# Performance work log

Measured on AMD Instinct MI355X. Metric: run time of the kernel, lower is better.

The kernel has to match this reference:

```python
import jax, jax.numpy as jnp
import numpy as np

N = 200000
SIZE = 16384
IN = 128
OUT = 128
HEADS = 4
SLOPE = 0.01  # nn.LeakyReLU default


def setup_inputs() -> dict:
    key = jax.random.key(0)
    ks = jax.random.split(key, 12)
    s = 0.05
    inp = {
        "fea": jax.random.normal(ks[0], (N, IN), jnp.float32),
        "cry_fea": jax.random.normal(ks[1], (SIZE, IN), jnp.float32),
        # MH_M: per-head MLP in->in->out (grouped conv1d k=1, groups=heads)
        "W_m1": jax.random.normal(ks[2], (HEADS, IN, IN), jnp.float32) * s,
        "b_m1": jax.random.normal(ks[3], (HEADS, IN), jnp.float32) * s,
        "W_m2": jax.random.normal(ks[4], (HEADS, OUT, IN), jnp.float32) * s,
        "b_m2": jax.random.normal(ks[5], (HEADS, OUT), jnp.float32) * s,
        # MH_A: per-head MLP 2*in->in->1 (scalar attention, vector_attention=False)
        "W_a1": jax.random.normal(ks[6], (HEADS, IN, 2 * IN), jnp.float32) * s,
        "b_a1": jax.random.normal(ks[7], (HEADS, IN), jnp.float32) * s,
        "W_a2": jax.random.normal(ks[8], (HEADS, 1, IN), jnp.float32) * s,
        "b_a2": jax.random.normal(ks[9], (HEADS, 1), jnp.float32) * s,
        "index": jnp.sort(jax.random.randint(ks[10], (N,), 0, SIZE, jnp.int32)),
        "size": SIZE,
    }
    return inp


def _leaky(x):
    return jnp.where(x >= 0, x, SLOPE * x)


def _mh_mlp(x, W1, b1, W2, b2):
    # x: [N, d_in]; per-head linear -> leaky -> linear. Returns [N, H, d_out].
    h = _leaky(jnp.einsum("ni,hoi->nho", x, W1) + b1)
    return jnp.einsum("nhi,hoi->nho", h, W2) + b2


def reference(fea, cry_fea, W_m1, b_m1, W_m2, b_m2, W_a1, b_a1, W_a2, b_a2, index, size):
    # message transform m: [N, H, OUT]
    m = _mh_mlp(fea, W_m1, b_m1, W_m2, b_m2)
    # attention input: concat(node fea, gathered crystal fea) -> [N, 2*IN]
    a_in = jnp.concatenate([fea, cry_fea[index]], axis=-1)
    alpha = _mh_mlp(a_in, W_a1, b_a1, W_a2, b_a2)  # [N, H, 1]
    # segment (per-crystal) softmax over nodes sharing the same index
    amax = jax.ops.segment_max(alpha, index, num_segments=size)
    amax = jnp.where(jnp.isfinite(amax), amax, 0.0)
    e = jnp.exp(alpha - amax[index])
    denom = jax.ops.segment_sum(e, index, num_segments=size)
    alpha = e / (denom[index] + 1e-16)
    # weighted scatter-add aggregation -> [size, H*OUT]
    out = jax.ops.segment_sum((alpha * m).reshape(-1, HEADS * OUT), index, num_segments=size)
    return out
```

## Files before the change

kernel.cpp:

```cpp
#include <hip/hip_runtime.h>

typedef __bf16 bf16x8 __attribute__((ext_vector_type(8)));
typedef float  f32x4  __attribute__((ext_vector_type(4)));
typedef unsigned int u32x4 __attribute__((ext_vector_type(4)));

#define MFMA(a, b, c) __builtin_amdgcn_mfma_f32_16x16x32_bf16((a), (b), (c), 0, 0, 0)

#define THREADS 1024
#define WAVES   16
#define CPW     4
#define CPB     64
#define MT      32

#define SEG_INTS  16416
#define SEG_BYTES (SEG_INTS * 4)
#define O_WM1 0
#define O_WM2 65536
#define O_WA1 131072
#define O_WA2 262144
#define W_ELEMS 262656
#define W_BYTES (W_ELEMS * 2)

#define LA1B 0
#define LM1B 32768
#define LM2B 65536

__device__ __forceinline__ bf16x8 cvt8(const float* pf) {
    float4 a = *(const float4*)pf, b = *(const float4*)(pf + 4);
    bf16x8 o;
    o[0] = (__bf16)a.x; o[1] = (__bf16)a.y; o[2] = (__bf16)a.z; o[3] = (__bf16)a.w;
    o[4] = (__bf16)b.x; o[5] = (__bf16)b.y; o[6] = (__bf16)b.z; o[7] = (__bf16)b.w;
    return o;
}

__device__ __forceinline__ unsigned pk2(float a, float b) {
    unsigned short ua = __builtin_bit_cast(unsigned short, (__bf16)a);
    unsigned short ub = __builtin_bit_cast(unsigned short, (__bf16)b);
    return (unsigned)ua | ((unsigned)ub << 16);
}

__device__ __forceinline__ int lower_bound(const int* __restrict__ a, int n, int v) {
    int lo = 0, hi = n;
    while (lo < hi) { int mid = (lo + hi) >> 1; if (a[mid] < v) lo = mid + 1; else hi = mid; }
    return lo;
}

__global__ __launch_bounds__(256) void prep3_kernel(
    const float* __restrict__ Wm1, const float* __restrict__ Wm2,
    const float* __restrict__ Wa1, const float* __restrict__ Wa2,
    const float* __restrict__ fea, const float* __restrict__ cry,
    const int* __restrict__ index, int N, int S,
    int segBlocks, int packBlocks, int cryBlocks,
    int* __restrict__ seg, __bf16* __restrict__ wb,
    __bf16* __restrict__ cryb, __bf16* __restrict__ feab, int full)
{
    int b = blockIdx.x;
    if (b < segBlocks) {
        int c = b * 256 + threadIdx.x;
        if (c <= S) seg[c] = lower_bound(index, N, c);
        return;
    }
    if (!full) return;
    b -= segBlocks;
    if (b < packBlocks) {
        int i8 = b * 256 + threadIdx.x;
        if (i8 >= W_ELEMS / 8) return;
        int i = i8 * 8;
        const float* src; int s;
        if      (i < O_WM2) { src = Wm1; s = i; }
        else if (i < O_WA1) { src = Wm2; s = i - O_WM2; }
        else if (i < O_WA2) { src = Wa1; s = i - O_WA1; }
        else                { src = Wa2; s = i - O_WA2; }
        *(bf16x8*)(wb + i) = cvt8(src + s);
        return;
    }
    b -= packBlocks;
    if (b < cryBlocks) {
        int i = b * 256 + threadIdx.x;
        if (i < S * 16) *(bf16x8*)(cryb + (size_t)i * 8) = cvt8(cry + (size_t)i * 8);
        return;
    }
    b -= cryBlocks;
    int i = b * 256 + threadIdx.x;
    if (i < N * 16) *(bf16x8*)(feab + (size_t)i * 8) = cvt8(fea + (size_t)i * 8);
}

template<bool WB, bool SEG, bool FB>
__global__ __launch_bounds__(THREADS) void fused6_kernel(
    const float* __restrict__ fea, const float* __restrict__ cry,
    const float* __restrict__ Wm1, const float* __restrict__ bm1,
    const float* __restrict__ Wm2, const float* __restrict__ bm2,
    const float* __restrict__ Wa1, const float* __restrict__ ba1,
    const float* __restrict__ Wa2, const float* __restrict__ ba2,
    const __bf16* __restrict__ wb, const int* __restrict__ seg,
    const __bf16* __restrict__ feab, const __bf16* __restrict__ cryb,
    const int* __restrict__ index, int N, int S, float* __restrict__ out)
{
    __shared__ __align__(16) __bf16 wlds[49152];
    __shared__ float crylds[WAVES][CPW][128];
    __shared__ float bm1lds[128];

    const int G = (S + CPB - 1) / CPB;
    int h, cg;
    if ((G & 7) == 0) {
        const int xcd = blockIdx.x & 7, j = blockIdx.x >> 3;
        h = j & 3; cg = xcd + 8 * (j >> 2);
    } else {
        h = blockIdx.x & 3; cg = blockIdx.x >> 2;
    }
    const int c0 = cg * CPB;
    const int t  = threadIdx.x;
    const int lane = t & 63, w = t >> 6, ml = lane & 15, q = lane >> 4;
    const int swzb = (ml & 7) << 4;
    const char* wbytes = (const char*)wlds;

#pragma unroll
    for (int i = 0; i < 6; i++) {
        const int cb = (t + i * THREADS) << 4;
        const int r = cb >> 15;
        const int local = cb & 32767;
        const int row = local >> 8;
        const int col8 = ((((local >> 4) & 15) ^ (row & 7)) << 3);
        bf16x8 v;
        if (r == 0) {
            if constexpr (WB) v = *(const bf16x8*)(wb + O_WA1 + (size_t)h * 32768 + row * 256 + col8);
            else              v = cvt8(Wa1 + (size_t)h * 32768 + (size_t)row * 256 + col8);
        } else if (r == 1) {
            if constexpr (WB) v = *(const bf16x8*)(wb + O_WM1 + (size_t)h * 16384 + row * 128 + col8);
            else              v = cvt8(Wm1 + (size_t)h * 16384 + (size_t)row * 128 + col8);
        } else {
            if constexpr (WB) v = *(const bf16x8*)(wb + O_WM2 + (size_t)h * 16384 + row * 128 + col8);
            else              v = cvt8(Wm2 + (size_t)h * 16384 + (size_t)row * 128 + col8);
        }
        *(bf16x8*)((char*)wlds + cb) = v;
    }
    if (t < 32) *(float4*)&bm1lds[t * 4] = *(const float4*)&bm1[h * 128 + t * 4];
    __syncthreads();

    const int cw0 = min(c0 + w * CPW, S);
    const int cw1 = min(cw0 + CPW, S);
    int start, end;
    if constexpr (SEG) { start = seg[cw0]; end = seg[cw1]; }
    else { start = lower_bound(index, N, cw0); end = lower_bound(index, N, cw1); }

    float ba1v[8], bb2[8], wa2v[8];
#pragma unroll
    for (int ot = 0; ot < 8; ot++) {
        ba1v[ot] = ba1[h * 128 + ot * 16 + ml];
        bb2[ot]  = bm2[h * 128 + ot * 16 + ml];
        wa2v[ot] = Wa2[h * 128 + ot * 16 + ml];
    }
    const float ba2v = ba2[h];

    {
        bf16x8 cf[4];
#pragma unroll
        for (int kk = 0; kk < 4; kk++) {
            bf16x8 z;
#pragma unroll
            for (int j = 0; j < 8; j++) z[j] = (__bf16)0.f;
            if (ml < CPW && cw0 + ml < S) {
                if constexpr (FB) z = *(const bf16x8*)(cryb + (size_t)(cw0 + ml) * 128 + kk * 32 + q * 8);
                else              z = cvt8(cry + (size_t)(cw0 + ml) * 128 + kk * 32 + q * 8);
            }
            cf[kk] = z;
        }
#pragma unroll
        for (int ot = 0; ot < 8; ot++) {
            f32x4 acc = {0.f, 0.f, 0.f, 0.f};
#pragma unroll
            for (int kk = 0; kk < 4; kk++) {
                bf16x8 B;
                size_t off = (size_t)h * 32768 + (size_t)(ot * 16 + ml) * 256 + 128 + kk * 32 + q * 8;
                if constexpr (WB) B = *(const bf16x8*)(wb + O_WA1 + off);
                else              B = cvt8(Wa1 + off);
                acc = MFMA(cf[kk], B, acc);
            }
            if (q == 0) {
#pragma unroll
                for (int r = 0; r < 4; r++) crylds[w][r][ot * 16 + ml] = acc[r];
            }
        }
    }

    float m_run = -1e30f, d_run = 0.f;
    float wacc[8] = {0.f,0.f,0.f,0.f,0.f,0.f,0.f,0.f};
    int cur_c = -1, emit_c = cw0;

    auto flushf = [&]() {
        float inv = 1.f / (d_run + 1e-16f);
        for (int z = emit_c; z < cur_c; z++)
            *(float2*)&out[(size_t)z * 512 + h * 128 + lane * 2] = make_float2(0.f, 0.f);
#pragma unroll
        for (int ot = 0; ot < 8; ot++) {
            float v = wacc[ot];
            v += __shfl_xor(v, 16);
            v += __shfl_xor(v, 32);
            if (q == 0) out[(size_t)cur_c * 512 + h * 128 + ot * 16 + ml] = v * inv;
            wacc[ot] = 0.f;
        }
        emit_c = cur_c + 1;
        m_run = -1e30f; d_run = 0.f;
    };

    for (int tb = start; tb < end; tb += MT) {
        int nv = end - tb; if (nv > MT) nv = MT;

        const int iv = (lane < nv) ? index[tb + lane] : cw0;

        unsigned long long bmask;
        {
            int ivp = __shfl(iv, lane > 0 ? lane - 1 : 0);
            bmask = __ballot(lane < nv && (lane == 0 || iv != ivp));
        }

        for (int s = 0; s < 2; s++) {
            const int lo = s * 16;
            if (lo >= nv) break;
            int hcnt = nv - lo; if (hcnt > 16) hcnt = 16;

            bf16x8 afh[4];
            {
                const int row = lo + ml;
                const bool val = row < nv;
#pragma unroll
                for (int kk = 0; kk < 4; kk++) {
                    bf16x8 z;
#pragma unroll
                    for (int j = 0; j < 8; j++) z[j] = (__bf16)0.f;
                    if (val) {
                        if constexpr (FB) z = *(const bf16x8*)(feab + (size_t)(tb + row) * 128 + kk * 32 + q * 8);
                        else              z = cvt8(fea + (size_t)(tb + row) * 128 + kk * 32 + q * 8);
                    }
                    afh[kk] = z;
                }
            }

            float lv4[4];
            {
                int cl4[4];
#pragma unroll
                for (int r = 0; r < 4; r++)
                    cl4[r] = __shfl(iv, lo + q * 4 + r) - cw0;
                float lsum[4] = {0.f, 0.f, 0.f, 0.f};
#pragma unroll
                for (int ot = 0; ot < 8; ot++) {
                    bf16x8 B[4];
#pragma unroll
                    for (int kk = 0; kk < 4; kk++)
                        B[kk] = *(const bf16x8*)(wbytes + LA1B + (ot * 16 + ml) * 256 + ((((kk * 4 + q) << 4)) ^ swzb));
                    const int oc = ot * 16 + ml;
                    f32x4 acc;
#pragma unroll
                    for (int r = 0; r < 4; r++) acc[r] = crylds[w][cl4[r]][oc];
#pragma unroll
                    for (int kk = 0; kk < 4; kk++) acc = MFMA(afh[kk], B[kk], acc);
#pragma unroll
                    for (int r = 0; r < 4; r++) {
                        float v = acc[r] + ba1v[ot]; v = v >= 0.f ? v : 0.01f * v;
                        lsum[r] += v * wa2v[ot];
                    }
                }
#pragma unroll
                for (int rr = 0; rr < 4; rr++) {
                    float x = lsum[rr];
                    x += __shfl_xor(x, 1); x += __shfl_xor(x, 2);
                    x += __shfl_xor(x, 4); x += __shfl_xor(x, 8);
                    lv4[rr] = x + ba2v;
                }
            }

            bf16x8 a2h[4];
#pragma unroll
            for (int kk = 0; kk < 4; kk++) {
                unsigned pw[2][2];
#pragma unroll
                for (int otl = 0; otl < 2; otl++) {
                    const int ot = kk * 2 + otl;
                    bf16x8 A[4];
#pragma unroll
                    for (int k4 = 0; k4 < 4; k4++)
                        A[k4] = *(const bf16x8*)(wbytes + LM1B + (ot * 16 + ml) * 256 + ((((k4 * 4 + q) << 4)) ^ swzb));
                    const float4 bq = *(const float4*)&bm1lds[ot * 16 + q * 4];
                    f32x4 acc = {0.f, 0.f, 0.f, 0.f};
#pragma unroll
                    for (int k4 = 0; k4 < 4; k4++) acc = MFMA(A[k4], afh[k4], acc);
                    float v0 = acc[0] + bq.x, v1 = acc[1] + bq.y;
                    float v2 = acc[2] + bq.z, v3 = acc[3] + bq.w;
                    v0 = v0 >= 0.f ? v0 : 0.01f * v0;  v1 = v1 >= 0.f ? v1 : 0.01f * v1;
                    v2 = v2 >= 0.f ? v2 : 0.01f * v2;  v3 = v3 >= 0.f ? v3 : 0.01f * v3;
                    pw[otl][0] = pk2(v0, v1);
                    pw[otl][1] = pk2(v2, v3);
                }
                const int srcLo = (((2 * q) & 3) << 4) + ml;
                const int srcHi = (((2 * q + 1) & 3) << 4) + ml;
                const bool hiSel = (q >> 1) & 1;
                unsigned l0a = (unsigned)__shfl((int)pw[0][0], srcLo);
                unsigned l0b = (unsigned)__shfl((int)pw[1][0], srcLo);
                unsigned l1a = (unsigned)__shfl((int)pw[0][1], srcLo);
                unsigned l1b = (unsigned)__shfl((int)pw[1][1], srcLo);
                unsigned h0a = (unsigned)__shfl((int)pw[0][0], srcHi);
                unsigned h0b = (unsigned)__shfl((int)pw[1][0], srcHi);
                unsigned h1a = (unsigned)__shfl((int)pw[0][1], srcHi);
                unsigned h1b = (unsigned)__shfl((int)pw[1][1], srcHi);
                u32x4 wv4u = { hiSel ? l0b : l0a, hiSel ? l1b : l1a,
                               hiSel ? h0b : h0a, hiSel ? h1b : h1a };
                a2h[kk] = __builtin_bit_cast(bf16x8, wv4u);
            }

            f32x4 acc2h[8];
#pragma unroll
            for (int ot = 0; ot < 8; ot++) {
                bf16x8 B[4];
#pragma unroll
                for (int kk = 0; kk < 4; kk++)
                    B[kk] = *(const bf16x8*)(wbytes + LM2B + (ot * 16 + ml) * 256 + ((((kk * 4 + q) << 4)) ^ swzb));
                f32x4 acc = {bb2[ot], bb2[ot], bb2[ot], bb2[ot]};
#pragma unroll
                for (int kk = 0; kk < 4; kk++) acc = MFMA(a2h[kk], B[kk], acc);
                acc2h[ot] = acc;
            }

            unsigned hm = (unsigned)((bmask >> lo) & 0xffffull) | 1u;
            if (hcnt < 16) hm &= (1u << hcnt) - 1u;
            while (hm) {
                int a = (int)__builtin_ctz(hm);
                hm &= hm - 1u;
                int b = hm ? (int)__builtin_ctz(hm) : hcnt;
                int c = __shfl(iv, lo + a);
                if (c != cur_c) {
                    if (cur_c >= 0) flushf();
                    cur_c = c;
                }
                float tmax = -1e30f;
#pragma unroll
                for (int rr = 0; rr < 4; rr++) {
                    int row = q * 4 + rr;
                    if (row >= a && row < b) tmax = fmaxf(tmax, lv4[rr]);
                }
                tmax = fmaxf(tmax, __shfl_xor(tmax, 16));
                tmax = fmaxf(tmax, __shfl_xor(tmax, 32));
                float m_new = fmaxf(m_run, tmax);
                float scf = __expf(m_run - m_new);
                d_run *= scf;
#pragma unroll
                for (int ot = 0; ot < 8; ot++) wacc[ot] *= scf;
                m_run = m_new;

                float wv4[4]; float dp = 0.f;
#pragma unroll
                for (int rr = 0; rr < 4; rr++) {
                    int row = q * 4 + rr;
                    float ww = (row >= a && row < b) ? __expf(lv4[rr] - m_run) : 0.f;
                    wv4[rr] = ww; dp += ww;
                }
                dp += __shfl_xor(dp, 16);
                dp += __shfl_xor(dp, 32);
                d_run += dp;
#pragma unroll
                for (int ot = 0; ot < 8; ot++) {
                    f32x4 acc = acc2h[ot];
                    wacc[ot] += wv4[0] * acc[0] + wv4[1] * acc[1]
                              + wv4[2] * acc[2] + wv4[3] * acc[3];
                }
            }
        }
    }

    if (cur_c >= 0) flushf();
    for (int z = emit_c; z < cw1; z++)
        *(float2*)&out[(size_t)z * 512 + h * 128 + lane * 2] = make_float2(0.f, 0.f);
}

extern "C" void kernel_launch(void* const* d_in, const int* in_sizes, int n_in,
                              void* d_out, int out_size, void* d_ws, size_t ws_size,
                              hipStream_t stream)
{
    const float* fea = (const float*)d_in[0];
    const float* cry = (const float*)d_in[1];
    const float* Wm1 = (const float*)d_in[2];
    const float* bm1 = (const float*)d_in[3];
    const float* Wm2 = (const float*)d_in[4];
    const float* bm2 = (const float*)d_in[5];
    const float* Wa1 = (const float*)d_in[6];
    const float* ba1 = (const float*)d_in[7];
    const float* Wa2 = (const float*)d_in[8];
    const float* ba2 = (const float*)d_in[9];
    const int* index = (const int*)d_in[10];

    const int N = in_sizes[0] / 128;
    const int S = out_size / 512;
    const int G = (S + CPB - 1) / CPB;
    const int grid = 4 * G;

    const int segBlocks  = (S + 1 + 255) / 256;
    const int packBlocks = (W_ELEMS / 8 + 255) / 256;
    const int cryBlocks  = (S * 16 + 255) / 256;
    const int feaBlocks  = (N * 16 + 255) / 256;
    const bool segFits = (S + 1) <= SEG_INTS;

    const size_t wOff   = (size_t)SEG_BYTES;
    const size_t cryOff = wOff + (size_t)W_BYTES;
    const size_t feaOff = cryOff + (size_t)S * 256;
    const size_t needSeg  = (size_t)SEG_BYTES;
    const size_t needFull = feaOff + (size_t)N * 256;

    if (segFits && ws_size >= needFull) {
        int* seg = (int*)d_ws;
        __bf16* wbp  = (__bf16*)((char*)d_ws + wOff);
        __bf16* cryb = (__bf16*)((char*)d_ws + cryOff);
        __bf16* feab = (__bf16*)((char*)d_ws + feaOff);
        prep3_kernel<<<segBlocks + packBlocks + cryBlocks + feaBlocks, 256, 0, stream>>>(
            Wm1, Wm2, Wa1, Wa2, fea, cry, index, N, S,
            segBlocks, packBlocks, cryBlocks, seg, wbp, cryb, feab, 1);
        fused6_kernel<true, true, true><<<grid, THREADS, 0, stream>>>(
            fea, cry, Wm1, bm1, Wm2, bm2, Wa1, ba1, Wa2, ba2,
            wbp, seg, feab, cryb, index, N, S, (float*)d_out);
    } else if (segFits && ws_size >= needSeg) {
        int* seg = (int*)d_ws;
        prep3_kernel<<<segBlocks, 256, 0, stream>>>(
            Wm1, Wm2, Wa1, Wa2, fea, cry, index, N, S,
            segBlocks, packBlocks, cryBlocks, seg, nullptr, nullptr, nullptr, 0);
        fused6_kernel<false, true, false><<<grid, THREADS, 0, stream>>>(
            fea, cry, Wm1, bm1, Wm2, bm2, Wa1, ba1, Wa2, ba2,
            nullptr, seg, nullptr, nullptr, index, N, S, (float*)d_out);
    } else {
        fused6_kernel<false, false, false><<<grid, THREADS, 0, stream>>>(
            fea, cry, Wm1, bm1, Wm2, bm2, Wa1, ba1, Wa2, ba2,
            nullptr, nullptr, nullptr, nullptr, index, N, S, (float*)d_out);
    }
}
```

Before: 461.1 us.

## Halve block size and stream Wa1 from global to fit two blocks per CU

Blocks shrink from 1024 to 512 threads with 32 crystals per block, and launch bounds now request 2 blocks per CU. To make that fit, the Wa1 node-half weights are no longer staged in LDS and are read directly from global memory (bf16 workspace or fp32 converted on the fly) inside the inner loop. The bm1 bias is also read from global instead of LDS. The aim is more resident waves to hide latency and less per-block weight staging. The cost is extra global/L2 traffic for Wa1 fragments in the hot loop and possible register pressure from the occupancy bound.

Result: slower. 576.9 us (+25.1%).

```diff
diff --git a/kernel.cpp b/kernel.cpp
--- a/kernel.cpp
+++ b/kernel.cpp
@@ -6,10 +6,10 @@
 
 #define MFMA(a, b, c) __builtin_amdgcn_mfma_f32_16x16x32_bf16((a), (b), (c), 0, 0, 0)
 
-#define THREADS 1024
-#define WAVES   16
+#define THREADS 512
+#define WAVES   8
 #define CPW     4
-#define CPB     64
+#define CPB     32
 #define MT      32
 
 #define SEG_INTS  16416
@@ -21,9 +21,8 @@
 #define W_ELEMS 262656
 #define W_BYTES (W_ELEMS * 2)
 
-#define LA1B 0
-#define LM1B 32768
-#define LM2B 65536
+#define LM1B 0
+#define LM2B 32768
 
 __device__ __forceinline__ bf16x8 cvt8(const float* pf) {
     float4 a = *(const float4*)pf, b = *(const float4*)(pf + 4);
@@ -43,6 +42,12 @@
     int lo = 0, hi = n;
     while (lo < hi) { int mid = (lo + hi) >> 1; if (a[mid] < v) lo = mid + 1; else hi = mid; }
     return lo;
+}
+
+template<bool WB>
+__device__ __forceinline__ bf16x8 wfrag(const __bf16* wb, const float* wf, size_t idx) {
+    if constexpr (WB) return *(const bf16x8*)(wb + idx);
+    else              return cvt8(wf + idx);
 }
 
 __global__ __launch_bounds__(256) void prep3_kernel(
@@ -86,7 +91,7 @@
 }
 
 template<bool WB, bool SEG, bool FB>
-__global__ __launch_bounds__(THREADS) void fused6_kernel(
+__global__ __launch_bounds__(THREADS, 2) void fused7_kernel(
     const float* __restrict__ fea, const float* __restrict__ cry,
     const float* __restrict__ Wm1, const float* __restrict__ bm1,
     const float* __restrict__ Wm2, const float* __restrict__ bm2,
@@ -96,9 +101,8 @@
     const __bf16* __restrict__ feab, const __bf16* __restrict__ cryb,
     const int* __restrict__ index, int N, int S, float* __restrict__ out)
 {
-    __shared__ __align__(16) __bf16 wlds[49152];
+    __shared__ __align__(16) __bf16 wlds[32768];
     __shared__ float crylds[WAVES][CPW][128];
-    __shared__ float bm1lds[128];
 
     const int G = (S + CPB - 1) / CPB;
     int h, cg;
@@ -115,7 +119,7 @@
     const char* wbytes = (const char*)wlds;
 
 #pragma unroll
-    for (int i = 0; i < 6; i++) {
+    for (int i = 0; i < 8; i++) {
         const int cb = (t + i * THREADS) << 4;
         const int r = cb >> 15;
         const int local = cb & 32767;
@@ -123,9 +127,6 @@
         const int col8 = ((((local >> 4) & 15) ^ (row & 7)) << 3);
         bf16x8 v;
         if (r == 0) {
-            if constexpr (WB) v = *(const bf16x8*)(wb + O_WA1 + (size_t)h * 32768 + row * 256 + col8);
-            else              v = cvt8(Wa1 + (size_t)h * 32768 + (size_t)row * 256 + col8);
-        } else if (r == 1) {
             if constexpr (WB) v = *(const bf16x8*)(wb + O_WM1 + (size_t)h * 16384 + row * 128 + col8);
             else              v = cvt8(Wm1 + (size_t)h * 16384 + (size_t)row * 128 + col8);
         } else {
@@ -134,7 +135,6 @@
         }
         *(bf16x8*)((char*)wlds + cb) = v;
     }
-    if (t < 32) *(float4*)&bm1lds[t * 4] = *(const float4*)&bm1[h * 128 + t * 4];
     __syncthreads();
 
     const int cw0 = min(c0 + w * CPW, S);
@@ -151,6 +151,7 @@
         wa2v[ot] = Wa2[h * 128 + ot * 16 + ml];
     }
     const float ba2v = ba2[h];
+    const float* bm1h = bm1 + h * 128;
 
     {
         bf16x8 cf[4];
@@ -167,15 +168,11 @@
         }
 #pragma unroll
         for (int ot = 0; ot < 8; ot++) {
+            size_t wrow = (size_t)h * 32768 + (size_t)(ot * 16 + ml) * 256;
             f32x4 acc = {0.f, 0.f, 0.f, 0.f};
 #pragma unroll
-            for (int kk = 0; kk < 4; kk++) {
-                bf16x8 B;
-                size_t off = (size_t)h * 32768 + (size_t)(ot * 16 + ml) * 256 + 128 + kk * 32 + q * 8;
-                if constexpr (WB) B = *(const bf16x8*)(wb + O_WA1 + off);
-                else              B = cvt8(Wa1 + off);
-                acc = MFMA(cf[kk], B, acc);
-            }
+            for (int kk = 0; kk < 4; kk++)
+                acc = MFMA(cf[kk], wfrag<WB>(wb + O_WA1, Wa1, wrow + 128 + kk * 32 + q * 8), acc);
             if (q == 0) {
 #pragma unroll
                 for (int r = 0; r < 4; r++) crylds[w][r][ot * 16 + ml] = acc[r];
@@ -245,16 +242,14 @@
                 float lsum[4] = {0.f, 0.f, 0.f, 0.f};
 #pragma unroll
                 for (int ot = 0; ot < 8; ot++) {
-                    bf16x8 B[4];
-#pragma unroll
-                    for (int kk = 0; kk < 4; kk++)
-                        B[kk] = *(const bf16x8*)(wbytes + LA1B + (ot * 16 + ml) * 256 + ((((kk * 4 + q) << 4)) ^ swzb));
+                    size_t wrow = (size_t)h * 32768 + (size_t)(ot * 16 + ml) * 256;
                     const int oc = ot * 16 + ml;
                     f32x4 acc;
 #pragma unroll
                     for (int r = 0; r < 4; r++) acc[r] = crylds[w][cl4[r]][oc];
 #pragma unroll
-                    for (int kk = 0; kk < 4; kk++) acc = MFMA(afh[kk], B[kk], acc);
+                    for (int kk = 0; kk < 4; kk++)
+                        acc = MFMA(afh[kk], wfrag<WB>(wb + O_WA1, Wa1, wrow + kk * 32 + q * 8), acc);
 #pragma unroll
                     for (int r = 0; r < 4; r++) {
                         float v = acc[r] + ba1v[ot]; v = v >= 0.f ? v : 0.01f * v;
@@ -281,7 +276,7 @@
 #pragma unroll
                     for (int k4 = 0; k4 < 4; k4++)
                         A[k4] = *(const bf16x8*)(wbytes + LM1B + (ot * 16 + ml) * 256 + ((((k4 * 4 + q) << 4)) ^ swzb));
-                    const float4 bq = *(const float4*)&bm1lds[ot * 16 + q * 4];
+                    const float4 bq = *(const float4*)&bm1h[ot * 16 + q * 4];
                     f32x4 acc = {0.f, 0.f, 0.f, 0.f};
 #pragma unroll
                     for (int k4 = 0; k4 < 4; k4++) acc = MFMA(A[k4], afh[k4], acc);
@@ -413,7 +408,7 @@
         prep3_kernel<<<segBlocks + packBlocks + cryBlocks + feaBlocks, 256, 0, stream>>>(
             Wm1, Wm2, Wa1, Wa2, fea, cry, index, N, S,
             segBlocks, packBlocks, cryBlocks, seg, wbp, cryb, feab, 1);
-        fused6_kernel<true, true, true><<<grid, THREADS, 0, stream>>>(
+        fused7_kernel<true, true, true><<<grid, THREADS, 0, stream>>>(
             fea, cry, Wm1, bm1, Wm2, bm2, Wa1, ba1, Wa2, ba2,
             wbp, seg, feab, cryb, index, N, S, (float*)d_out);
     } else if (segFits && ws_size >= needSeg) {
@@ -421,11 +416,11 @@
         prep3_kernel<<<segBlocks, 256, 0, stream>>>(
             Wm1, Wm2, Wa1, Wa2, fea, cry, index, N, S,
             segBlocks, packBlocks, cryBlocks, seg, nullptr, nullptr, nullptr, 0);
-        fused6_kernel<false, true, false><<<grid, THREADS, 0, stream>>>(
+        fused7_kernel<false, true, false><<<grid, THREADS, 0, stream>>>(
             fea, cry, Wm1, bm1, Wm2, bm2, Wa1, ba1, Wa2, ba2,
             nullptr, seg, nullptr, nullptr, index, N, S, (float*)d_out);
     } else {
-        fused6_kernel<false, false, false><<<grid, THREADS, 0, stream>>>(
+        fused7_kernel<false, false, false><<<grid, THREADS, 0, stream>>>(
             fea, cry, Wm1, bm1, Wm2, bm2, Wa1, ba1, Wa2, ba2,
             nullptr, nullptr, nullptr, nullptr, index, N, S, (float*)d_out);
     }
```
